# Kernel tuning notes

Hardware: AMD Instinct MI355X
Metric: run time of the kernel (lower is better)

The kernel has to match this reference:

```python
import jax, jax.numpy as jnp
import numpy as np

VOCAB, D = 100000, 128
B, V, S = 1024, 20, 30
N_CLASS = 20
H0, H1 = 256, 128  # hidden_dims


def setup_inputs() -> dict:
    key = jax.random.key(0)
    ks = jax.random.split(key, 10)
    diag_idx = jax.random.randint(ks[0], (B, V, S), 0, VOCAB, dtype=jnp.int32)
    proc_idx = jax.random.randint(ks[1], (B, V, S), 0, VOCAB, dtype=jnp.int32)
    embedding = jax.random.normal(ks[2], (VOCAB, D), dtype=jnp.float32)
    # fc0: (2D -> H0), fc1: (H0 -> H1), fc2: (H1 -> n_class); torch Linear layout [out,in]
    W0 = jax.random.normal(ks[3], (H0, 2 * D), dtype=jnp.float32) * (1.0 / np.sqrt(2 * D))
    b0 = jnp.zeros((H0,), dtype=jnp.float32)
    W1 = jax.random.normal(ks[4], (H1, H0), dtype=jnp.float32) * (1.0 / np.sqrt(H0))
    b1 = jnp.zeros((H1,), dtype=jnp.float32)
    W2 = jax.random.normal(ks[5], (N_CLASS, H1), dtype=jnp.float32) * (1.0 / np.sqrt(H1))
    b2 = jnp.zeros((N_CLASS,), dtype=jnp.float32)
    return {"diag_idx": diag_idx, "proc_idx": proc_idx, "embedding": embedding,
            "W0": W0, "b0": b0, "W1": W1, "b1": b1, "W2": W2, "b2": b2}


def _pool(embedding, idx):
    # gather [B,V,S,D], mean over set dim S, sum over visit dim V -> [B,D]
    e = embedding[idx]
    return e.mean(axis=2).sum(axis=1)


def reference(diag_idx, proc_idx, embedding, W0, b0, W1, b1, W2, b2):
    d = _pool(embedding, diag_idx)            # [B, D]
    p = _pool(embedding, proc_idx)            # [B, D]
    x = jnp.concatenate([d, p], axis=-1)      # [B, 2D]
    out = x @ W0.T + b0                        # fc_layers[0]
    out = jax.nn.relu(out) @ W1.T + b1         # relu applied before each subsequent layer
    out = jax.nn.relu(out) @ W2.T + b2
    return out                                  # [B, n_class]
```

## Files before the change

### kernel.cpp

```cpp
#include <hip/hip_runtime.h>

#define BATCH 1024
#define VS 600
#define D 128
#define H0 256
#define H1 128
#define NCLASS 20
#define CAP 128
#define SPB 4


__global__ __launch_bounds__(256) void bucket_kernel(
    const int* __restrict__ diag_idx, const int* __restrict__ proc_idx,
    unsigned short* __restrict__ lists, int* __restrict__ counts)
{
    __shared__ int cnt[16];
    const int s = blockIdx.x, tid = threadIdx.x;
    if (tid < 16) cnt[tid] = 0;
    __syncthreads();

    const int* dsrc = diag_idx + s * VS;
    const int* psrc = proc_idx + s * VS;
    for (int i = tid; i < VS; i += 256) {
        const int r = dsrc[i];
        const int b = r & 7;
        const int pos = atomicAdd(&cnt[b], 1);
        if (pos < CAP) lists[(s * 16 + b) * CAP + pos] = (unsigned short)(r >> 3);
        const int r2 = psrc[i];
        const int b2 = 8 + (r2 & 7);
        const int pos2 = atomicAdd(&cnt[b2], 1);
        if (pos2 < CAP) lists[(s * 16 + b2) * CAP + pos2] = (unsigned short)(r2 >> 3);
    }
    __syncthreads();
    if (tid < 16) counts[s * 16 + tid] = min(cnt[tid], CAP);
}

__global__ __launch_bounds__(256) void gather_partial_kernel(
    const unsigned short* __restrict__ lists, const int* __restrict__ counts,
    const float* __restrict__ emb, float* __restrict__ part)
{
    __shared__ unsigned short lq[2 * CAP];
    __shared__ int c2[2];
    __shared__ __attribute__((aligned(16))) float red[8][D];

    const int bid = blockIdx.x;
    const int x   = bid & 7;
    const int s   = bid >> 3;
    const int tid = threadIdx.x;

    if (tid < 2) c2[tid] = counts[s * 16 + tid * 8 + x];
    if (tid < CAP)           lq[tid] = lists[(s * 16 + x) * CAP + tid];
    else if (tid < 2 * CAP)  lq[tid] = lists[(s * 16 + 8 + x) * CAP + (tid - CAP)];
    __syncthreads();

    const int grp = tid >> 5, lane = tid & 31;
    const int pool = grp >> 2, sub = grp & 3;
    const int cnt = c2[pool];
    const unsigned short* lp = lq + pool * CAP;
    float4 acc = make_float4(0.f, 0.f, 0.f, 0.f);
    #pragma unroll 4
    for (int i = sub; i < cnt; i += 4) {
        const int row = ((int)lp[i] << 3) | x;
        const float4 e = ((const float4*)(emb + row * D))[lane];
        acc.x += e.x; acc.y += e.y; acc.z += e.z; acc.w += e.w;
    }
    ((float4*)red[grp])[lane] = acc;
    __syncthreads();

    {
        const int p = tid >> 7, d = tid & 127;
        const float v = red[p*4+0][d] + red[p*4+1][d] + red[p*4+2][d] + red[p*4+3][d];
        part[(x * BATCH + s) * (2 * D) + tid] = v * (1.0f / 30.0f);
    }
}

__global__ __launch_bounds__(512) void mlp_kernel(
    const float* __restrict__ part,
    const float* __restrict__ W0, const float* __restrict__ b0,
    const float* __restrict__ W1, const float* __restrict__ b1,
    const float* __restrict__ W2, const float* __restrict__ b2,
    float* __restrict__ out)
{
    __shared__ __attribute__((aligned(16))) float xs [SPB][2 * D];
    __shared__ __attribute__((aligned(16))) float h0s[SPB][H0];
    __shared__ __attribute__((aligned(16))) float h1s[SPB][H1];

    const int s0 = blockIdx.x * SPB, tid = threadIdx.x;

    #pragma unroll
    for (int t = tid; t < SPB * 2 * D; t += 512) {
        const int j = t >> 8, d = t & 255;
        float v = 0.f;
        #pragma unroll
        for (int xp = 0; xp < 8; ++xp)
            v += part[(xp * BATCH + s0 + j) * (2 * D) + d];
        xs[j][d] = v;
    }
    __syncthreads();

    {
        const int row = tid >> 1, half = tid & 1;
        const float4* wrow = (const float4*)(W0 + row * (2 * D) + half * D);
        const int xoff = half * (D / 4);
        float a[SPB];
        #pragma unroll
        for (int j = 0; j < SPB; ++j) a[j] = 0.f;
        #pragma unroll 4
        for (int k = 0; k < 32; ++k) {
            const float4 w = wrow[k];
            #pragma unroll
            for (int j = 0; j < SPB; ++j) {
                const float4 xx = ((const float4*)xs[j])[xoff + k];
                a[j] += w.x * xx.x + w.y * xx.y + w.z * xx.z + w.w * xx.w;
            }
        }
        #pragma unroll
        for (int j = 0; j < SPB; ++j) {
            a[j] += __shfl_xor(a[j], 1);
            if (!half) h0s[j][row] = fmaxf(a[j] + b0[row], 0.f);
        }
    }
    __syncthreads();

    {
        const int row = tid >> 2, q = tid & 3;
        const float4* wrow = (const float4*)(W1 + row * H0 + q * 64);
        const int hoff = q * 16;
        float a[SPB];
        #pragma unroll
        for (int j = 0; j < SPB; ++j) a[j] = 0.f;
        #pragma unroll 4
        for (int k = 0; k < 16; ++k) {
            const float4 w = wrow[k];
            #pragma unroll
            for (int j = 0; j < SPB; ++j) {
                const float4 hh = ((const float4*)h0s[j])[hoff + k];
                a[j] += w.x * hh.x + w.y * hh.y + w.z * hh.z + w.w * hh.w;
            }
        }
        #pragma unroll
        for (int j = 0; j < SPB; ++j) {
            a[j] += __shfl_xor(a[j], 1);
            a[j] += __shfl_xor(a[j], 2);
            if (!q) h1s[j][row] = fmaxf(a[j] + b1[row], 0.f);
        }
    }
    __syncthreads();

    if (tid < NCLASS * 16) {
        const int row = tid >> 4, q = (tid >> 2) & 3, j = tid & 3;
        const float4* wrow = (const float4*)(W2 + row * H1 + q * 32);
        const float4* hv   = (const float4*)(h1s[j] + q * 32);
        float a = 0.f;
        #pragma unroll
        for (int k = 0; k < 8; ++k) {
            const float4 w = wrow[k], hh = hv[k];
            a += w.x * hh.x + w.y * hh.y + w.z * hh.z + w.w * hh.w;
        }
        a += __shfl_xor(a, 4);
        a += __shfl_xor(a, 8);
        if (!q) out[(s0 + j) * NCLASS + row] = a + b2[row];
    }
}

extern "C" void kernel_launch(void* const* d_in, const int* in_sizes, int n_in,
                              void* d_out, int out_size, void* d_ws, size_t ws_size,
                              hipStream_t stream) {
    const int*   diag_idx = (const int*)d_in[0];
    const int*   proc_idx = (const int*)d_in[1];
    const float* emb      = (const float*)d_in[2];
    const float* W0       = (const float*)d_in[3];
    const float* b0       = (const float*)d_in[4];
    const float* W1       = (const float*)d_in[5];
    const float* b1       = (const float*)d_in[6];
    const float* W2       = (const float*)d_in[7];
    const float* b2       = (const float*)d_in[8];
    float* out = (float*)d_out;

    char* ws = (char*)d_ws;
    float*          part   = (float*)ws;
    unsigned short* lists  = (unsigned short*)(ws + 8*1024*1024);
    int*            counts = (int*)(ws + 12*1024*1024);

    bucket_kernel<<<BATCH, 256, 0, stream>>>(diag_idx, proc_idx, lists, counts);
    gather_partial_kernel<<<8 * BATCH, 256, 0, stream>>>(lists, counts, emb, part);
    mlp_kernel<<<BATCH / SPB, 512, 0, stream>>>(part, W0, b0, W1, b1, W2, b2, out);
}
```

Baseline: 153.9 us.

## Split embedding gather into four passes over row-residue buckets for cache locality

```diff
diff --git a/kernel.cpp b/kernel.cpp
--- a/kernel.cpp
+++ b/kernel.cpp
@@ -6,7 +6,9 @@
 #define H0 256
 #define H1 128
 #define NCLASS 20
-#define CAP 128
+#define NB 32
+#define PASSES 4
+#define CAP 48
 #define SPB 4
 
 
@@ -14,30 +16,30 @@
     const int* __restrict__ diag_idx, const int* __restrict__ proc_idx,
     unsigned short* __restrict__ lists, int* __restrict__ counts)
 {
-    __shared__ int cnt[16];
+    __shared__ int cnt[2 * NB];
     const int s = blockIdx.x, tid = threadIdx.x;
-    if (tid < 16) cnt[tid] = 0;
+    if (tid < 2 * NB) cnt[tid] = 0;
     __syncthreads();
 
     const int* dsrc = diag_idx + s * VS;
     const int* psrc = proc_idx + s * VS;
     for (int i = tid; i < VS; i += 256) {
         const int r = dsrc[i];
-        const int b = r & 7;
+        const int b = r & (NB - 1);
         const int pos = atomicAdd(&cnt[b], 1);
-        if (pos < CAP) lists[(s * 16 + b) * CAP + pos] = (unsigned short)(r >> 3);
+        if (pos < CAP) lists[((s * 2 + 0) * NB + b) * CAP + pos] = (unsigned short)(r >> 5);
         const int r2 = psrc[i];
-        const int b2 = 8 + (r2 & 7);
-        const int pos2 = atomicAdd(&cnt[b2], 1);
-        if (pos2 < CAP) lists[(s * 16 + b2) * CAP + pos2] = (unsigned short)(r2 >> 3);
+        const int b2 = r2 & (NB - 1);
+        const int pos2 = atomicAdd(&cnt[NB + b2], 1);
+        if (pos2 < CAP) lists[((s * 2 + 1) * NB + b2) * CAP + pos2] = (unsigned short)(r2 >> 5);
     }
     __syncthreads();
-    if (tid < 16) counts[s * 16 + tid] = min(cnt[tid], CAP);
+    if (tid < 2 * NB) counts[s * 2 * NB + tid] = min(cnt[tid], CAP);
 }
 
 __global__ __launch_bounds__(256) void gather_partial_kernel(
     const unsigned short* __restrict__ lists, const int* __restrict__ counts,
-    const float* __restrict__ emb, float* __restrict__ part)
+    const float* __restrict__ emb, float* __restrict__ part, const int p)
 {
     __shared__ unsigned short lq[2 * CAP];
     __shared__ int c2[2];
@@ -47,10 +49,11 @@
     const int x   = bid & 7;
     const int s   = bid >> 3;
     const int tid = threadIdx.x;
+    const int b   = p * 8 + x;
 
-    if (tid < 2) c2[tid] = counts[s * 16 + tid * 8 + x];
-    if (tid < CAP)           lq[tid] = lists[(s * 16 + x) * CAP + tid];
-    else if (tid < 2 * CAP)  lq[tid] = lists[(s * 16 + 8 + x) * CAP + (tid - CAP)];
+    if (tid < 2) c2[tid] = counts[s * 2 * NB + tid * NB + b];
+    if (tid < CAP)           lq[tid] = lists[((s * 2 + 0) * NB + b) * CAP + tid];
+    else if (tid < 2 * CAP)  lq[tid] = lists[((s * 2 + 1) * NB + b) * CAP + (tid - CAP)];
     __syncthreads();
 
     const int grp = tid >> 5, lane = tid & 31;
@@ -58,9 +61,8 @@
     const int cnt = c2[pool];
     const unsigned short* lp = lq + pool * CAP;
     float4 acc = make_float4(0.f, 0.f, 0.f, 0.f);
-    #pragma unroll 4
     for (int i = sub; i < cnt; i += 4) {
-        const int row = ((int)lp[i] << 3) | x;
+        const int row = ((int)lp[i] << 5) | b;
         const float4 e = ((const float4*)(emb + row * D))[lane];
         acc.x += e.x; acc.y += e.y; acc.z += e.z; acc.w += e.w;
     }
@@ -68,9 +70,12 @@
     __syncthreads();
 
     {
-        const int p = tid >> 7, d = tid & 127;
-        const float v = red[p*4+0][d] + red[p*4+1][d] + red[p*4+2][d] + red[p*4+3][d];
-        part[(x * BATCH + s) * (2 * D) + tid] = v * (1.0f / 30.0f);
+        const int pl = tid >> 7, d = tid & 127;
+        const float v = (red[pl*4+0][d] + red[pl*4+1][d] + red[pl*4+2][d] + red[pl*4+3][d])
+                        * (1.0f / 30.0f);
+        const int idx = (x * BATCH + s) * (2 * D) + tid;
+        if (p == 0) part[idx] = v;
+        else        part[idx] += v;
     }
 }
 
@@ -180,9 +185,10 @@
     char* ws = (char*)d_ws;
     float*          part   = (float*)ws;
     unsigned short* lists  = (unsigned short*)(ws + 8*1024*1024);
-    int*            counts = (int*)(ws + 12*1024*1024);
+    int*            counts = (int*)(ws + 14*1024*1024);
 
     bucket_kernel<<<BATCH, 256, 0, stream>>>(diag_idx, proc_idx, lists, counts);
-    gather_partial_kernel<<<8 * BATCH, 256, 0, stream>>>(lists, counts, emb, part);
+    for (int p = 0; p < PASSES; ++p)
+        gather_partial_kernel<<<8 * BATCH, 256, 0, stream>>>(lists, counts, emb, part, p);
     mlp_kernel<<<BATCH / SPB, 512, 0, stream>>>(part, W0, b0, W1, b1, W2, b2, out);
 }
```

Measured after the change: 176.3 us. +14.5%, slower.
